# Kernel tuning notes

Hardware: AMD Instinct MI355X
Metric: run time of the kernel (lower is better)

Reference implementation:

```python
import jax, jax.numpy as jnp
import numpy as np

N = 50000   # nodes
E = 600000  # edges (avg degree 12)
F = 16      # raw node features
P = 32      # n_channels_preproc
C = 128     # n_channels
L = 6       # n_gnn_layers
LBL = 2     # n_labels


def _dense_init(k, fan_in, shape):
    return (jax.random.normal(k, shape, jnp.float32) / np.float32(np.sqrt(fan_in)))


def setup_inputs() -> dict:
    key = jax.random.key(0)
    ks = jax.random.split(key, 12)
    return {
        "x": jax.random.normal(ks[0], (N, F), jnp.float32),
        "edge_src": jax.random.randint(ks[1], (E,), 0, N, dtype=jnp.int32),
        "edge_dst": jax.random.randint(ks[2], (E,), 0, N, dtype=jnp.int32),
        "edge_weight": jax.random.uniform(ks[3], (E,), jnp.float32),  # normalized-adjacency values
        "preproc_W": _dense_init(ks[4], F, (F, P)), "preproc_b": jnp.zeros((P,), jnp.float32),
        "fc_in1_W": _dense_init(ks[5], P, (P, C)), "fc_in1_b": jnp.zeros((C,), jnp.float32),
        "fc_in2_W": _dense_init(ks[6], P, (P, C)), "fc_in2_b": jnp.zeros((C,), jnp.float32),
        "gcn_W": _dense_init(ks[7], C, (L, C, C)), "gcn_b": jnp.zeros((L, C), jnp.float32),
        "fcg_W": _dense_init(ks[8], 2 * C, (L, 2 * C, C)), "fcg_b": jnp.zeros((L, C), jnp.float32),
        "last1_W": _dense_init(ks[9], 2 * C, (2 * C, C)), "last1_b": jnp.zeros((C,), jnp.float32),
        "last2_W": _dense_init(ks[10], C, (C, LBL)), "last2_b": jnp.zeros((LBL,), jnp.float32),
    }


def reference(x, edge_src, edge_dst, edge_weight,
              preproc_W, preproc_b, fc_in1_W, fc_in1_b, fc_in2_W, fc_in2_b,
              gcn_W, gcn_b, fcg_W, fcg_b, last1_W, last1_b, last2_W, last2_b):
    relu = jax.nn.relu
    h = relu(x @ preproc_W + preproc_b)                      # preproc Dense
    node_id = relu(h @ fc_in1_W + fc_in1_b)                  # node identity branch
    h = relu(h @ fc_in2_W + fc_in2_b)

    def layer(h, params):
        W, b, Wf, bf = params
        # GCNConv: act(A_hat @ (h @ W) + b), A_hat as COO edge list
        hw = h @ W                                           # [N, C]
        msg = hw[edge_src] * edge_weight[:, None]            # [E, C]
        agg = jax.ops.segment_sum(msg, edge_dst, num_segments=N)
        g = relu(agg + b)
        merged = jnp.concatenate([node_id, g], axis=-1)      # [N, 2C]
        return relu(merged @ Wf + bf), None                  # dropout = identity (eval)

    h, _ = jax.lax.scan(layer, h, (gcn_W, gcn_b, fcg_W, fcg_b))

    merged = jnp.concatenate([node_id, h], axis=-1)
    h = relu(merged @ last1_W + last1_b)
    return jax.nn.sigmoid(h @ last2_W + last2_b)             # [N, n_labels]
```

## Files before the change

kernel.cpp:

```cpp
#include <hip/hip_runtime.h>
#include <cstddef>
#include <cstdint>

#define NN 50000
#define NE 600000
#define NB 391

typedef __attribute__((ext_vector_type(8))) short bf16x8;
typedef __attribute__((ext_vector_type(4))) float f32x4;

#define SWZ(x) (((x) ^ ((x) >> 2)) & 3)

__device__ __forceinline__ float bf2f(ushort u) {
    return __uint_as_float(((uint32_t)u) << 16);
}
__device__ __forceinline__ ushort f2bf(float f) {
    uint32_t b = __float_as_uint(f);
    return (ushort)((b + 0x7FFF + ((b >> 16) & 1)) >> 16);
}

__global__ __launch_bounds__(256)
void convert_weights(const float* __restrict__ f1W, const float* __restrict__ f2W,
                     const float* __restrict__ gW, const float* __restrict__ fgW,
                     const float* __restrict__ l1W, ushort* __restrict__ wt)
{
    int i = blockIdx.x * 256 + threadIdx.x;
    if (i >= 335872) return;
    float v;
    if (i < 4096) {
        int c = i >> 5, k = i & 31;
        v = f1W[k * 128 + c];
    } else if (i < 8192) {
        int j = i - 4096; int c = j >> 5, k = j & 31;
        v = f2W[k * 128 + c];
    } else if (i < 8192 + 98304) {
        int j = i - 8192; int l = j >> 14, r = j & 16383;
        int c = r >> 7, k = r & 127;
        v = gW[l * 16384 + k * 128 + c];
    } else if (i < 8192 + 98304 + 196608) {
        int j = i - (8192 + 98304); int l = j >> 15, r = j & 32767;
        int c = r >> 8, k = r & 255;
        v = fgW[l * 32768 + k * 128 + c];
    } else {
        int j = i - (8192 + 98304 + 196608);
        int c = j >> 8, k = j & 255;
        v = l1W[k * 128 + c];
    }
    wt[i] = f2bf(v);
}

__global__ __launch_bounds__(256)
void preproc_kernel(const float* __restrict__ x, const float* __restrict__ W,
                    const float* __restrict__ b, ushort* __restrict__ out)
{
    __shared__ float Wl[512];
    __shared__ float bl[32];
    int tx = threadIdx.x;
    Wl[tx]       = W[tx];
    Wl[tx + 256] = W[tx + 256];
    if (tx < 32) bl[tx] = b[tx];
    __syncthreads();
    int n = blockIdx.x * 256 + tx;
    if (n >= NN) return;
    float xr[16];
    const float4* xp = (const float4*)(x + (size_t)n * 16);
#pragma unroll
    for (int q = 0; q < 4; ++q) {
        float4 v = xp[q];
        xr[q*4+0]=v.x; xr[q*4+1]=v.y; xr[q*4+2]=v.z; xr[q*4+3]=v.w;
    }
    float acc[32];
#pragma unroll
    for (int c = 0; c < 32; ++c) acc[c] = bl[c];
#pragma unroll
    for (int k = 0; k < 16; ++k)
#pragma unroll
        for (int c = 0; c < 32; ++c)
            acc[c] = fmaf(xr[k], Wl[k*32+c], acc[c]);
    ushort4* op = (ushort4*)(out + (size_t)n * 32);
#pragma unroll
    for (int q = 0; q < 8; ++q) {
        ushort4 v;
        v.x = f2bf(fmaxf(acc[q*4+0], 0.f));
        v.y = f2bf(fmaxf(acc[q*4+1], 0.f));
        v.z = f2bf(fmaxf(acc[q*4+2], 0.f));
        v.w = f2bf(fmaxf(acc[q*4+3], 0.f));
        op[q] = v;
    }
}

__global__ __launch_bounds__(128)
void gemm_mfma(const ushort* __restrict__ A1, int K1,
               const ushort* __restrict__ Wt, const float* __restrict__ bias,
               ushort* __restrict__ out, int nrows)
{
    __shared__ ushort Atile[64 * 32];
    __shared__ ushort Btile[128 * 32];
    const int tx   = threadIdx.x;
    const int wave = tx >> 6;
    const int lane = tx & 63;
    const int bm   = blockIdx.x * 64;
    const int Ktot = K1;

    const int rs  = lane >> 2;
    const int chn = (lane & 3) ^ SWZ(rs);
    const int m    = lane & 15;
    const int quad = lane >> 4;
    const int slot = quad ^ SWZ(m);

    f32x4 acc0[8], acc1[8];
#pragma unroll
    for (int t = 0; t < 8; ++t) {
        acc0[t] = (f32x4){0.f, 0.f, 0.f, 0.f};
        acc1[t] = (f32x4){0.f, 0.f, 0.f, 0.f};
    }

    for (int kk = 0; kk < Ktot; kk += 32) {
#pragma unroll
        for (int i = 0; i < 2; ++i) {
            int seg = wave + 2 * i;
            int row = seg * 16 + rs;
            int ar  = bm + row; if (ar >= nrows) ar = nrows - 1;
            __builtin_amdgcn_global_load_lds(
                (const __attribute__((address_space(1))) void*)
                    (A1 + (size_t)ar * K1 + kk + chn * 8),
                (__attribute__((address_space(3))) void*)(Atile + seg * 512),
                16, 0, 0);
        }
#pragma unroll
        for (int i = 0; i < 4; ++i) {
            int seg = wave + 2 * i;
            int col = seg * 16 + rs;
            __builtin_amdgcn_global_load_lds(
                (const __attribute__((address_space(1))) void*)
                    (Wt + (size_t)col * Ktot + kk + chn * 8),
                (__attribute__((address_space(3))) void*)(Btile + seg * 512),
                16, 0, 0);
        }
        __syncthreads();
        bf16x8 af0 = *(const bf16x8*)(Atile + (wave * 32 + m) * 32 + slot * 8);
        bf16x8 af1 = *(const bf16x8*)(Atile + (wave * 32 + 16 + m) * 32 + slot * 8);
#pragma unroll
        for (int t = 0; t < 8; ++t) {
            bf16x8 bfr = *(const bf16x8*)(Btile + (t * 16 + m) * 32 + slot * 8);
            acc0[t] = __builtin_amdgcn_mfma_f32_16x16x32_bf16(af0, bfr, acc0[t], 0, 0, 0);
            acc1[t] = __builtin_amdgcn_mfma_f32_16x16x32_bf16(af1, bfr, acc1[t], 0, 0, 0);
        }
        __syncthreads();
    }

#pragma unroll
    for (int half = 0; half < 2; ++half) {
        const int orow0 = bm + wave * 32 + half * 16 + quad * 4;
#pragma unroll
        for (int t = 0; t < 8; ++t) {
            int col = t * 16 + m;
            float bb = bias[col];
            f32x4 a = half ? acc1[t] : acc0[t];
#pragma unroll
            for (int r = 0; r < 4; ++r) {
                int row = orow0 + r;
                if (row < nrows)
                    out[(size_t)row * 128 + col] = f2bf(fmaxf(a[r] + bb, 0.f));
            }
        }
    }
}

__global__ __launch_bounds__(128)
void gemm_fused(const ushort* __restrict__ A1, int K1,
                const ushort* __restrict__ A2, int K2,
                const ushort* __restrict__ Wt, const float* __restrict__ bias,
                const ushort* __restrict__ Wg,
                ushort* __restrict__ out_hw, int nrows)
{
    __shared__ ushort Atile[64 * 32];
    __shared__ ushort Btile[128 * 32];
    __shared__ ushort Xt[64 * 128];
    const int tx   = threadIdx.x;
    const int wave = tx >> 6;
    const int lane = tx & 63;
    const int bm   = blockIdx.x * 64;
    const int Ktot = K1 + K2;

    const int rs  = lane >> 2;
    const int chn = (lane & 3) ^ SWZ(rs);
    const int m    = lane & 15;
    const int quad = lane >> 4;
    const int slot = quad ^ SWZ(m);

    f32x4 acc0[8], acc1[8];
#pragma unroll
    for (int t = 0; t < 8; ++t) {
        acc0[t] = (f32x4){0.f, 0.f, 0.f, 0.f};
        acc1[t] = (f32x4){0.f, 0.f, 0.f, 0.f};
    }

    for (int kk = 0; kk < Ktot; kk += 32) {
        const ushort* asrc; int astr, kl;
        if (kk < K1) { asrc = A1; astr = K1; kl = kk; }
        else         { asrc = A2; astr = K2; kl = kk - K1; }
#pragma unroll
        for (int i = 0; i < 2; ++i) {
            int seg = wave + 2 * i;
            int row = seg * 16 + rs;
            int ar  = bm + row; if (ar >= nrows) ar = nrows - 1;
            __builtin_amdgcn_global_load_lds(
                (const __attribute__((address_space(1))) void*)
                    (asrc + (size_t)ar * astr + kl + chn * 8),
                (__attribute__((address_space(3))) void*)(Atile + seg * 512),
                16, 0, 0);
        }
#pragma unroll
        for (int i = 0; i < 4; ++i) {
            int seg = wave + 2 * i;
            int col = seg * 16 + rs;
            __builtin_amdgcn_global_load_lds(
                (const __attribute__((address_space(1))) void*)
                    (Wt + (size_t)col * Ktot + kk + chn * 8),
                (__attribute__((address_space(3))) void*)(Btile + seg * 512),
                16, 0, 0);
        }
        __syncthreads();
        bf16x8 af0 = *(const bf16x8*)(Atile + (wave * 32 + m) * 32 + slot * 8);
        bf16x8 af1 = *(const bf16x8*)(Atile + (wave * 32 + 16 + m) * 32 + slot * 8);
#pragma unroll
        for (int t = 0; t < 8; ++t) {
            bf16x8 bfr = *(const bf16x8*)(Btile + (t * 16 + m) * 32 + slot * 8);
            acc0[t] = __builtin_amdgcn_mfma_f32_16x16x32_bf16(af0, bfr, acc0[t], 0, 0, 0);
            acc1[t] = __builtin_amdgcn_mfma_f32_16x16x32_bf16(af1, bfr, acc1[t], 0, 0, 0);
        }
        __syncthreads();
    }

#pragma unroll
    for (int half = 0; half < 2; ++half) {
        int rbase = wave * 32 + half * 16 + quad * 4;
#pragma unroll
        for (int t = 0; t < 8; ++t) {
            int col = t * 16 + m;
            float bb = bias[col];
            int c32 = col >> 5, within = col & 7, ks = (col >> 3) & 3;
            f32x4 a = half ? acc1[t] : acc0[t];
#pragma unroll
            for (int r = 0; r < 4; ++r) {
                int row = rbase + r;
                int pos = ks ^ SWZ(row & 15);
                Xt[row * 128 + c32 * 32 + pos * 8 + within] =
                    f2bf(fmaxf(a[r] + bb, 0.f));
            }
        }
    }
#pragma unroll
    for (int t = 0; t < 8; ++t) {
        acc0[t] = (f32x4){0.f, 0.f, 0.f, 0.f};
        acc1[t] = (f32x4){0.f, 0.f, 0.f, 0.f};
    }
    __syncthreads();

    for (int c32 = 0; c32 < 4; ++c32) {
        int kk = c32 * 32;
#pragma unroll
        for (int i = 0; i < 4; ++i) {
            int seg = wave + 2 * i;
            int col = seg * 16 + rs;
            __builtin_amdgcn_global_load_lds(
                (const __attribute__((address_space(1))) void*)
                    (Wg + (size_t)col * 128 + kk + chn * 8),
                (__attribute__((address_space(3))) void*)(Btile + seg * 512),
                16, 0, 0);
        }
        __syncthreads();
        bf16x8 af0 = *(const bf16x8*)(Xt + (wave * 32 + m) * 128 + kk + slot * 8);
        bf16x8 af1 = *(const bf16x8*)(Xt + (wave * 32 + 16 + m) * 128 + kk + slot * 8);
#pragma unroll
        for (int t = 0; t < 8; ++t) {
            bf16x8 bfr = *(const bf16x8*)(Btile + (t * 16 + m) * 32 + slot * 8);
            acc0[t] = __builtin_amdgcn_mfma_f32_16x16x32_bf16(af0, bfr, acc0[t], 0, 0, 0);
            acc1[t] = __builtin_amdgcn_mfma_f32_16x16x32_bf16(af1, bfr, acc1[t], 0, 0, 0);
        }
        __syncthreads();
    }

#pragma unroll
    for (int half = 0; half < 2; ++half) {
        const int orow0 = bm + wave * 32 + half * 16 + quad * 4;
#pragma unroll
        for (int t = 0; t < 8; ++t) {
            int col = t * 16 + m;
            f32x4 a = half ? acc1[t] : acc0[t];
#pragma unroll
            for (int r = 0; r < 4; ++r) {
                int row = orow0 + r;
                if (row < nrows)
                    out_hw[(size_t)row * 128 + col] = f2bf(a[r]);
            }
        }
    }
}

__global__ __launch_bounds__(128)
void gemm_last(const ushort* __restrict__ nid, const ushort* __restrict__ agg,
               const ushort* __restrict__ Wt, const float* __restrict__ bias5,
               const ushort* __restrict__ Wl1, const float* __restrict__ l1b,
               const float* __restrict__ l2W, const float* __restrict__ l2b,
               float* __restrict__ out, int nrows)
{
    __shared__ ushort Atile[64 * 32];
    __shared__ ushort Btile[128 * 32];
    __shared__ ushort Xt[64 * 128];
    __shared__ float  w2s[256];
    const int tx   = threadIdx.x;
    const int wave = tx >> 6;
    const int lane = tx & 63;
    const int bm   = blockIdx.x * 64;

    w2s[tx]       = l2W[tx];
    w2s[tx + 128] = l2W[tx + 128];

    const int rs  = lane >> 2;
    const int chn = (lane & 3) ^ SWZ(rs);
    const int m    = lane & 15;
    const int quad = lane >> 4;
    const int slot = quad ^ SWZ(m);

    f32x4 acc0[8], acc1[8];
#pragma unroll
    for (int t = 0; t < 8; ++t) {
        acc0[t] = (f32x4){0.f, 0.f, 0.f, 0.f};
        acc1[t] = (f32x4){0.f, 0.f, 0.f, 0.f};
    }

    for (int kk = 0; kk < 256; kk += 32) {
        const ushort* asrc; int kl;
        if (kk < 128) { asrc = nid; kl = kk; }
        else          { asrc = agg; kl = kk - 128; }
#pragma unroll
        for (int i = 0; i < 2; ++i) {
            int seg = wave + 2 * i;
            int row = seg * 16 + rs;
            int ar  = bm + row; if (ar >= nrows) ar = nrows - 1;
            __builtin_amdgcn_global_load_lds(
                (const __attribute__((address_space(1))) void*)
                    (asrc + (size_t)ar * 128 + kl + chn * 8),
                (__attribute__((address_space(3))) void*)(Atile + seg * 512),
                16, 0, 0);
        }
#pragma unroll
        for (int i = 0; i < 4; ++i) {
            int seg = wave + 2 * i;
            int col = seg * 16 + rs;
            __builtin_amdgcn_global_load_lds(
                (const __attribute__((address_space(1))) void*)
                    (Wt + (size_t)col * 256 + kk + chn * 8),
                (__attribute__((address_space(3))) void*)(Btile + seg * 512),
                16, 0, 0);
        }
        __syncthreads();
        bf16x8 af0 = *(const bf16x8*)(Atile + (wave * 32 + m) * 32 + slot * 8);
        bf16x8 af1 = *(const bf16x8*)(Atile + (wave * 32 + 16 + m) * 32 + slot * 8);
#pragma unroll
        for (int t = 0; t < 8; ++t) {
            bf16x8 bfr = *(const bf16x8*)(Btile + (t * 16 + m) * 32 + slot * 8);
            acc0[t] = __builtin_amdgcn_mfma_f32_16x16x32_bf16(af0, bfr, acc0[t], 0, 0, 0);
            acc1[t] = __builtin_amdgcn_mfma_f32_16x16x32_bf16(af1, bfr, acc1[t], 0, 0, 0);
        }
        __syncthreads();
    }

#pragma unroll
    for (int half = 0; half < 2; ++half) {
        int rbase = wave * 32 + half * 16 + quad * 4;
#pragma unroll
        for (int t = 0; t < 8; ++t) {
            int col = t * 16 + m;
            float bb = bias5[col];
            int c32 = col >> 5, within = col & 7, ks = (col >> 3) & 3;
            f32x4 a = half ? acc1[t] : acc0[t];
#pragma unroll
            for (int r = 0; r < 4; ++r) {
                int row = rbase + r;
                int pos = ks ^ SWZ(row & 15);
                Xt[row * 128 + c32 * 32 + pos * 8 + within] =
                    f2bf(fmaxf(a[r] + bb, 0.f));
            }
        }
    }
#pragma unroll
    for (int t = 0; t < 8; ++t) {
        acc0[t] = (f32x4){0.f, 0.f, 0.f, 0.f};
        acc1[t] = (f32x4){0.f, 0.f, 0.f, 0.f};
    }
    __syncthreads();

    for (int c8 = 0; c8 < 8; ++c8) {
        int kk = c8 * 32;
        if (c8 < 4) {
#pragma unroll
            for (int i = 0; i < 2; ++i) {
                int seg = wave + 2 * i;
                int row = seg * 16 + rs;
                int ar  = bm + row; if (ar >= nrows) ar = nrows - 1;
                __builtin_amdgcn_global_load_lds(
                    (const __attribute__((address_space(1))) void*)
                        (nid + (size_t)ar * 128 + kk + chn * 8),
                    (__attribute__((address_space(3))) void*)(Atile + seg * 512),
                    16, 0, 0);
            }
        }
#pragma unroll
        for (int i = 0; i < 4; ++i) {
            int seg = wave + 2 * i;
            int col = seg * 16 + rs;
            __builtin_amdgcn_global_load_lds(
                (const __attribute__((address_space(1))) void*)
                    (Wl1 + (size_t)col * 256 + kk + chn * 8),
                (__attribute__((address_space(3))) void*)(Btile + seg * 512),
                16, 0, 0);
        }
        __syncthreads();
        bf16x8 af0, af1;
        if (c8 < 4) {
            af0 = *(const bf16x8*)(Atile + (wave * 32 + m) * 32 + slot * 8);
            af1 = *(const bf16x8*)(Atile + (wave * 32 + 16 + m) * 32 + slot * 8);
        } else {
            int ko = (c8 - 4) * 32;
            af0 = *(const bf16x8*)(Xt + (wave * 32 + m) * 128 + ko + slot * 8);
            af1 = *(const bf16x8*)(Xt + (wave * 32 + 16 + m) * 128 + ko + slot * 8);
        }
#pragma unroll
        for (int t = 0; t < 8; ++t) {
            bf16x8 bfr = *(const bf16x8*)(Btile + (t * 16 + m) * 32 + slot * 8);
            acc0[t] = __builtin_amdgcn_mfma_f32_16x16x32_bf16(af0, bfr, acc0[t], 0, 0, 0);
            acc1[t] = __builtin_amdgcn_mfma_f32_16x16x32_bf16(af1, bfr, acc1[t], 0, 0, 0);
        }
        __syncthreads();
    }

    float bb[8];
#pragma unroll
    for (int t = 0; t < 8; ++t) bb[t] = l1b[t * 16 + m];
    float b20 = l2b[0], b21 = l2b[1];
#pragma unroll
    for (int half = 0; half < 2; ++half) {
#pragma unroll
        for (int r = 0; r < 4; ++r) {
            float p0 = 0.f, p1 = 0.f;
#pragma unroll
            for (int t = 0; t < 8; ++t) {
                int col = t * 16 + m;
                f32x4 a = half ? acc1[t] : acc0[t];
                float v = fmaxf(a[r] + bb[t], 0.f);
                p0 = fmaf(v, w2s[col * 2 + 0], p0);
                p1 = fmaf(v, w2s[col * 2 + 1], p1);
            }
#pragma unroll
            for (int mask = 1; mask < 16; mask <<= 1) {
                p0 += __shfl_xor(p0, mask);
                p1 += __shfl_xor(p1, mask);
            }
            if (m == 0) {
                int row = bm + wave * 32 + half * 16 + quad * 4 + r;
                if (row < nrows) {
                    out[(size_t)row * 2 + 0] = 1.f / (1.f + __expf(-(p0 + b20)));
                    out[(size_t)row * 2 + 1] = 1.f / (1.f + __expf(-(p1 + b21)));
                }
            }
        }
    }
}


__global__ __launch_bounds__(256)
void bhist_kernel(const int* __restrict__ dst, int* __restrict__ bcnt)
{
    __shared__ int h[NB];
    int tx = threadIdx.x;
    for (int i = tx; i < NB; i += 256) h[i] = 0;
    __syncthreads();
    int e0 = blockIdx.x * 1024;
#pragma unroll
    for (int k = 0; k < 4; ++k) {
        int e = e0 + k * 256 + tx;
        if (e < NE) atomicAdd(&h[dst[e] >> 7], 1);
    }
    __syncthreads();
    for (int i = tx; i < NB; i += 256)
        if (h[i]) atomicAdd(&bcnt[i], h[i]);
}

__global__ __launch_bounds__(512)
void bscan_kernel(const int* __restrict__ bcnt, int* __restrict__ bbase,
                  int* __restrict__ bcur)
{
    __shared__ int buf[512];
    int t = threadIdx.x;
    int v = (t < NB) ? bcnt[t] : 0;
    buf[t] = v;
    __syncthreads();
    for (int s = 1; s < 512; s <<= 1) {
        int u = (t >= s) ? buf[t - s] : 0;
        __syncthreads();
        buf[t] += u;
        __syncthreads();
    }
    if (t < NB) {
        int ex = buf[t] - v;
        bbase[t] = ex;
        bcur[t]  = ex;
    }
    if (t == 0) bbase[NB] = NE;
}

__global__ __launch_bounds__(256)
void pass1_kernel(const int* __restrict__ src, const int* __restrict__ dst,
                  const float* __restrict__ w, int* __restrict__ bcur,
                  unsigned int* __restrict__ stage_pk,
                  unsigned char* __restrict__ stage_dl)
{
    __shared__ int cnt[NB];
    __shared__ int gbase[NB];
    int tx = threadIdx.x;
    for (int i = tx; i < NB; i += 256) cnt[i] = 0;
    __syncthreads();
    int e0 = blockIdx.x * 1024;
    int myd[4], myrank[4];
    unsigned int mypk[4];
#pragma unroll
    for (int k = 0; k < 4; ++k) {
        int e = e0 + k * 256 + tx;
        if (e < NE) {
            int d = dst[e];
            myd[k]    = d;
            mypk[k]   = (unsigned int)src[e] | ((unsigned int)f2bf(w[e]) << 17);
            myrank[k] = atomicAdd(&cnt[d >> 7], 1);
        } else {
            myd[k] = -1;
        }
    }
    __syncthreads();
    for (int i = tx; i < NB; i += 256)
        gbase[i] = cnt[i] ? atomicAdd(&bcur[i], cnt[i]) : 0;
    __syncthreads();
#pragma unroll
    for (int k = 0; k < 4; ++k) {
        if (myd[k] >= 0) {
            int p = gbase[myd[k] >> 7] + myrank[k];
            stage_pk[p] = mypk[k];
            stage_dl[p] = (unsigned char)(myd[k] & 127);
        }
    }
}

__global__ __launch_bounds__(256)
void pass2_kernel(const unsigned int* __restrict__ stage_pk,
                  const unsigned char* __restrict__ stage_dl,
                  const int* __restrict__ bbase,
                  unsigned int* __restrict__ esw, int* __restrict__ off)
{
    __shared__ int h[128];
    __shared__ int lofs[128];
    int b    = blockIdx.x;
    int tx   = threadIdx.x;
    int base = bbase[b];
    int cnt  = bbase[b + 1] - base;
    if (tx < 128) h[tx] = 0;
    __syncthreads();
    for (int i = tx; i < cnt; i += 256)
        atomicAdd(&h[stage_dl[base + i]], 1);
    __syncthreads();
    if (tx == 0) {
        int run = 0;
        for (int i = 0; i < 128; ++i) { lofs[i] = run; run += h[i]; }
    }
    __syncthreads();
    int node0 = b * 128;
    if (tx < 128) {
        int n = node0 + tx;
        if (n < NN) off[n] = base + lofs[tx];
        h[tx] = 0;
    }
    if (b == NB - 1 && tx == 0) off[NN] = NE;
    __syncthreads();
    for (int i = tx; i < cnt; i += 256) {
        int d = stage_dl[base + i];
        int r = atomicAdd(&h[d], 1);
        esw[base + lofs[d] + r] = stage_pk[base + i];
    }
}

__global__ __launch_bounds__(256)
void gather_agg(const ushort* __restrict__ hw,
                const unsigned int* __restrict__ esw,
                const int* __restrict__ off, const float* __restrict__ gbias,
                ushort* __restrict__ agg)
{
    const int g    = blockIdx.x * 4 + (threadIdx.x >> 6);
    const int lane = threadIdx.x & 63;
    int n = g * 8;
    if (n >= NN) return;
    int n_end = n + 8; if (n_end > NN) n_end = NN;
    const int base = off[n];
    const int end  = off[n_end];
    int nb = off[n + 1];
    const ushort* hp = hw + lane * 2;
    const float g0 = gbias[lane * 2], g1 = gbias[lane * 2 + 1];
    float a0 = 0.f, a1 = 0.f;

    for (int chunk = base; chunk < end; chunk += 64) {
        int idx = chunk + lane;
        int pk = (idx < end) ? (int)esw[idx] : 0;
        int cnt = end - chunk; if (cnt > 64) cnt = 64;
        int cnt8 = (cnt + 7) & ~7;
        for (int j = 0; j < cnt8; j += 8) {
            int pp[8];
            unsigned int rv[8];
#pragma unroll
            for (int k = 0; k < 8; ++k)
                pp[k] = __builtin_amdgcn_readlane(pk, j + k);
#pragma unroll
            for (int k = 0; k < 8; ++k)
                rv[k] = *(const unsigned int*)(hp + (size_t)(pp[k] & 0x1FFFF) * 128);
#pragma unroll
            for (int k = 0; k < 8; ++k) {
                int e = chunk + j + k;
                while (e == nb) {
                    unsigned int o = (unsigned int)f2bf(fmaxf(a0 + g0, 0.f)) |
                                     ((unsigned int)f2bf(fmaxf(a1 + g1, 0.f)) << 16);
                    *(unsigned int*)(agg + (size_t)n * 128 + lane * 2) = o;
                    a0 = 0.f; a1 = 0.f;
                    ++n;
                    nb = (n < n_end) ? off[n + 1] : 0x7fffffff;
                }
                float w = bf2f((ushort)((unsigned int)pp[k] >> 17));
                a0 = fmaf(bf2f((ushort)(rv[k] & 0xffff)), w, a0);
                a1 = fmaf(bf2f((ushort)(rv[k] >> 16)),    w, a1);
            }
        }
    }
    while (n < n_end) {
        unsigned int o = (unsigned int)f2bf(fmaxf(a0 + g0, 0.f)) |
                         ((unsigned int)f2bf(fmaxf(a1 + g1, 0.f)) << 16);
        *(unsigned int*)(agg + (size_t)n * 128 + lane * 2) = o;
        a0 = 0.f; a1 = 0.f;
        ++n;
    }
}

extern "C" void kernel_launch(void* const* d_in, const int* in_sizes, int n_in,
                              void* d_out, int out_size, void* d_ws, size_t ws_size,
                              hipStream_t stream)
{
    const float* x    = (const float*)d_in[0];
    const int*   esrc = (const int*)  d_in[1];
    const int*   edst = (const int*)  d_in[2];
    const float* ew   = (const float*)d_in[3];
    const float* preW = (const float*)d_in[4];
    const float* preb = (const float*)d_in[5];
    const float* f1W  = (const float*)d_in[6];
    const float* f1b  = (const float*)d_in[7];
    const float* f2W  = (const float*)d_in[8];
    const float* f2b  = (const float*)d_in[9];
    const float* gW   = (const float*)d_in[10];
    const float* gb   = (const float*)d_in[11];
    const float* fgW  = (const float*)d_in[12];
    const float* fgb  = (const float*)d_in[13];
    const float* l1W  = (const float*)d_in[14];
    const float* l1b  = (const float*)d_in[15];
    const float* l2W  = (const float*)d_in[16];
    const float* l2b  = (const float*)d_in[17];
    float* out = (float*)d_out;

    ushort* wt   = (ushort*)d_ws;
    ushort* wf1  = wt;
    ushort* wf2  = wf1 + 4096;
    ushort* wg   = wf2 + 4096;
    ushort* wfg  = wg  + 98304;
    ushort* wl1  = wfg + 196608;
    ushort* h0b  = wl1 + 32768;
    ushort* nidb = h0b  + (size_t)NN * 32;
    ushort* hwb  = nidb + (size_t)NN * 128;
    ushort* aggb = hwb  + (size_t)NN * 128;
    ushort* endu = aggb + (size_t)NN * 128;
    unsigned int* esw      = (unsigned int*)(((uintptr_t)endu + 15) & ~(uintptr_t)15);
    unsigned int* stage_pk = esw + NE;
    int*          bcnt     = (int*)(stage_pk + NE);
    int*          bbase    = bcnt + NB + 1;
    int*          bcur     = bbase + NB + 1;
    int*          off      = bcur + NB + 1;
    unsigned char* stage_dl = (unsigned char*)(off + NN + 2);

    const int gblocks = (NN + 63) / 64;
    const int eblocks = (NE + 1023) / 1024;
    const int ngroups = (NN + 7) / 8;
    const int wblocks = (ngroups + 3) / 4;

    convert_weights<<<(335872 + 255) / 256, 256, 0, stream>>>(f1W, f2W, gW, fgW, l1W, wt);

    hipMemsetAsync(bcnt, 0, (size_t)NB * sizeof(int), stream);
    bhist_kernel<<<eblocks, 256, 0, stream>>>(edst, bcnt);
    bscan_kernel<<<1, 512, 0, stream>>>(bcnt, bbase, bcur);
    pass1_kernel<<<eblocks, 256, 0, stream>>>(esrc, edst, ew, bcur, stage_pk, stage_dl);
    pass2_kernel<<<NB, 256, 0, stream>>>(stage_pk, stage_dl, bbase, esw, off);

    preproc_kernel<<<(NN + 255) / 256, 256, 0, stream>>>(x, preW, preb, h0b);
    gemm_mfma<<<gblocks, 128, 0, stream>>>(h0b, 32, wf1, f1b, nidb, NN);
    gemm_fused<<<gblocks, 128, 0, stream>>>(h0b, 32, nullptr, 0, wf2, f2b,
                                            wg, hwb, NN);
    for (int l = 0; l < 6; ++l) {
        gather_agg<<<wblocks, 256, 0, stream>>>(hwb, esw, off,
                                                gb + (size_t)l * 128, aggb);
        if (l < 5) {
            gemm_fused<<<gblocks, 128, 0, stream>>>(nidb, 128, aggb, 128,
                                                    wfg + (size_t)l * 32768,
                                                    fgb + (size_t)l * 128,
                                                    wg + (size_t)(l + 1) * 16384,
                                                    hwb, NN);
        }
    }
    gemm_last<<<gblocks, 128, 0, stream>>>(nidb, aggb,
                                           wfg + (size_t)5 * 32768,
                                           fgb + (size_t)5 * 128,
                                           wl1, l1b, l2W, l2b, out, NN);
}
```

Baseline: 428.1 us.

## Fuse edge gather-aggregation into the per-layer GEMM via LDS staging

The separate gather_agg kernel is removed. Each GEMM block now aggregates neighbour messages for its own 64 rows straight into a swizzled LDS tile, which then serves as the second half of the K dimension. hw buffers are ping-ponged because the gather reads the previous layer's hw while the new hw is written. This removes a launch per layer and the global write and read of the agg tensor, at the cost of 16KB more LDS per block (lower occupancy) and gather work spread over only 128-thread blocks, with two waves each handling 32 nodes serially.

```diff
diff --git a/kernel.cpp b/kernel.cpp
--- a/kernel.cpp
+++ b/kernel.cpp
@@ -169,7 +169,6 @@
 
 __global__ __launch_bounds__(128)
 void gemm_fused(const ushort* __restrict__ A1, int K1,
-                const ushort* __restrict__ A2, int K2,
                 const ushort* __restrict__ Wt, const float* __restrict__ bias,
                 const ushort* __restrict__ Wg,
                 ushort* __restrict__ out_hw, int nrows)
@@ -181,7 +180,7 @@
     const int wave = tx >> 6;
     const int lane = tx & 63;
     const int bm   = blockIdx.x * 64;
-    const int Ktot = K1 + K2;
+    const int Ktot = K1;
 
     const int rs  = lane >> 2;
     const int chn = (lane & 3) ^ SWZ(rs);
@@ -197,9 +196,6 @@
     }
 
     for (int kk = 0; kk < Ktot; kk += 32) {
-        const ushort* asrc; int astr, kl;
-        if (kk < K1) { asrc = A1; astr = K1; kl = kk; }
-        else         { asrc = A2; astr = K2; kl = kk - K1; }
 #pragma unroll
         for (int i = 0; i < 2; ++i) {
             int seg = wave + 2 * i;
@@ -207,7 +203,7 @@
             int ar  = bm + row; if (ar >= nrows) ar = nrows - 1;
             __builtin_amdgcn_global_load_lds(
                 (const __attribute__((address_space(1))) void*)
-                    (asrc + (size_t)ar * astr + kl + chn * 8),
+                    (A1 + (size_t)ar * K1 + kk + chn * 8),
                 (__attribute__((address_space(3))) void*)(Atile + seg * 512),
                 16, 0, 0);
         }
@@ -299,24 +295,78 @@
     }
 }
 
+#define GATHER_TO_LDS(AggL)                                                     \
+    {                                                                           \
+        int n0 = bm + wave * 32;                                                \
+        if (n0 < nrows) {                                                       \
+            int n_end = n0 + 32; if (n_end > nrows) n_end = nrows;              \
+            const int base = off[n0];                                           \
+            const int end  = off[n_end];                                        \
+            int nb = off[n0 + 1];                                               \
+            int n  = n0;                                                        \
+            const ushort* hp = hw + lane * 2;                                   \
+            const float g0 = gbias[lane * 2], g1 = gbias[lane * 2 + 1];         \
+            const int c32w = lane >> 4, ksw = (lane >> 2) & 3, wi2 = lane & 3;  \
+            float a0 = 0.f, a1 = 0.f;                                           \
+            for (int chunk = base; chunk < end; chunk += 64) {                  \
+                int idx = chunk + lane;                                         \
+                int pk = (idx < end) ? (int)esw[idx] : 0;                       \
+                int cnt = end - chunk; if (cnt > 64) cnt = 64;                  \
+                int cnt8 = (cnt + 7) & ~7;                                      \
+                for (int j = 0; j < cnt8; j += 8) {                             \
+                    int pp[8]; unsigned int rv[8];                              \
+                    _Pragma("unroll")                                           \
+                    for (int k = 0; k < 8; ++k)                                 \
+                        pp[k] = __builtin_amdgcn_readlane(pk, j + k);           \
+                    _Pragma("unroll")                                           \
+                    for (int k = 0; k < 8; ++k)                                 \
+                        rv[k] = *(const unsigned int*)(hp + (size_t)(pp[k] & 0x1FFFF) * 128); \
+                    _Pragma("unroll")                                           \
+                    for (int k = 0; k < 8; ++k) {                               \
+                        int e = chunk + j + k;                                  \
+                        while (e == nb) {                                       \
+                            int row = n - bm;                                   \
+                            int pos = ksw ^ SWZ(row & 15);                      \
+                            unsigned int o = (unsigned int)f2bf(fmaxf(a0 + g0, 0.f)) | \
+                                ((unsigned int)f2bf(fmaxf(a1 + g1, 0.f)) << 16);\
+                            ((unsigned int*)(AggL))[row * 64 + c32w * 16 + pos * 4 + wi2] = o; \
+                            a0 = 0.f; a1 = 0.f; ++n;                            \
+                            nb = (n < n_end) ? off[n + 1] : 0x7fffffff;         \
+                        }                                                       \
+                        float w = bf2f((ushort)((unsigned int)pp[k] >> 17));    \
+                        a0 = fmaf(bf2f((ushort)(rv[k] & 0xffff)), w, a0);       \
+                        a1 = fmaf(bf2f((ushort)(rv[k] >> 16)),    w, a1);       \
+                    }                                                           \
+                }                                                               \
+            }                                                                   \
+            while (n < n_end) {                                                 \
+                int row = n - bm;                                               \
+                int pos = ksw ^ SWZ(row & 15);                                  \
+                unsigned int o = (unsigned int)f2bf(fmaxf(a0 + g0, 0.f)) |      \
+                    ((unsigned int)f2bf(fmaxf(a1 + g1, 0.f)) << 16);            \
+                ((unsigned int*)(AggL))[row * 64 + c32w * 16 + pos * 4 + wi2] = o; \
+                a0 = 0.f; a1 = 0.f; ++n;                                        \
+            }                                                                   \
+        }                                                                       \
+    }
+
 __global__ __launch_bounds__(128)
-void gemm_last(const ushort* __restrict__ nid, const ushort* __restrict__ agg,
-               const ushort* __restrict__ Wt, const float* __restrict__ bias5,
-               const ushort* __restrict__ Wl1, const float* __restrict__ l1b,
-               const float* __restrict__ l2W, const float* __restrict__ l2b,
-               float* __restrict__ out, int nrows)
+void gemm_fused_g(const ushort* __restrict__ hw,
+                  const unsigned int* __restrict__ esw,
+                  const int* __restrict__ off, const float* __restrict__ gbias,
+                  const ushort* __restrict__ nid,
+                  const ushort* __restrict__ Wt, const float* __restrict__ bias,
+                  const ushort* __restrict__ Wg,
+                  ushort* __restrict__ out_hw, int nrows)
 {
     __shared__ ushort Atile[64 * 32];
     __shared__ ushort Btile[128 * 32];
     __shared__ ushort Xt[64 * 128];
-    __shared__ float  w2s[256];
+    __shared__ ushort AggL[64 * 128];
     const int tx   = threadIdx.x;
     const int wave = tx >> 6;
     const int lane = tx & 63;
     const int bm   = blockIdx.x * 64;
-
-    w2s[tx]       = l2W[tx];
-    w2s[tx + 128] = l2W[tx + 128];
 
     const int rs  = lane >> 2;
     const int chn = (lane & 3) ^ SWZ(rs);
@@ -324,6 +374,9 @@
     const int quad = lane >> 4;
     const int slot = quad ^ SWZ(m);
 
+    GATHER_TO_LDS(AggL)
+    __syncthreads();
+
     f32x4 acc0[8], acc1[8];
 #pragma unroll
     for (int t = 0; t < 8; ++t) {
@@ -332,70 +385,7 @@
     }
 
     for (int kk = 0; kk < 256; kk += 32) {
-        const ushort* asrc; int kl;
-        if (kk < 128) { asrc = nid; kl = kk; }
-        else          { asrc = agg; kl = kk - 128; }
-#pragma unroll
-        for (int i = 0; i < 2; ++i) {
-            int seg = wave + 2 * i;
-            int row = seg * 16 + rs;
-            int ar  = bm + row; if (ar >= nrows) ar = nrows - 1;
-            __builtin_amdgcn_global_load_lds(
-                (const __attribute__((address_space(1))) void*)
-                    (asrc + (size_t)ar * 128 + kl + chn * 8),
-                (__attribute__((address_space(3))) void*)(Atile + seg * 512),
-                16, 0, 0);
-        }
-#pragma unroll
-        for (int i = 0; i < 4; ++i) {
-            int seg = wave + 2 * i;
-            int col = seg * 16 + rs;
-            __builtin_amdgcn_global_load_lds(
-                (const __attribute__((address_space(1))) void*)
-                    (Wt + (size_t)col * 256 + kk + chn * 8),
-                (__attribute__((address_space(3))) void*)(Btile + seg * 512),
-                16, 0, 0);
-        }
-        __syncthreads();
-        bf16x8 af0 = *(const bf16x8*)(Atile + (wave * 32 + m) * 32 + slot * 8);
-        bf16x8 af1 = *(const bf16x8*)(Atile + (wave * 32 + 16 + m) * 32 + slot * 8);
-#pragma unroll
-        for (int t = 0; t < 8; ++t) {
-            bf16x8 bfr = *(const bf16x8*)(Btile + (t * 16 + m) * 32 + slot * 8);
-            acc0[t] = __builtin_amdgcn_mfma_f32_16x16x32_bf16(af0, bfr, acc0[t], 0, 0, 0);
-            acc1[t] = __builtin_amdgcn_mfma_f32_16x16x32_bf16(af1, bfr, acc1[t], 0, 0, 0);
-        }
-        __syncthreads();
-    }
-
-#pragma unroll
-    for (int half = 0; half < 2; ++half) {
-        int rbase = wave * 32 + half * 16 + quad * 4;
-#pragma unroll
-        for (int t = 0; t < 8; ++t) {
-            int col = t * 16 + m;
-            float bb = bias5[col];
-            int c32 = col >> 5, within = col & 7, ks = (col >> 3) & 3;
-            f32x4 a = half ? acc1[t] : acc0[t];
-#pragma unroll
-            for (int r = 0; r < 4; ++r) {
-                int row = rbase + r;
-                int pos = ks ^ SWZ(row & 15);
-                Xt[row * 128 + c32 * 32 + pos * 8 + within] =
-                    f2bf(fmaxf(a[r] + bb, 0.f));
-            }
-        }
-    }
-#pragma unroll
-    for (int t = 0; t < 8; ++t) {
-        acc0[t] = (f32x4){0.f, 0.f, 0.f, 0.f};
-        acc1[t] = (f32x4){0.f, 0.f, 0.f, 0.f};
-    }
-    __syncthreads();
-
-    for (int c8 = 0; c8 < 8; ++c8) {
-        int kk = c8 * 32;
-        if (c8 < 4) {
+        if (kk < 128) {
 #pragma unroll
             for (int i = 0; i < 2; ++i) {
                 int seg = wave + 2 * i;
@@ -414,6 +404,223 @@
             int col = seg * 16 + rs;
             __builtin_amdgcn_global_load_lds(
                 (const __attribute__((address_space(1))) void*)
+                    (Wt + (size_t)col * 256 + kk + chn * 8),
+                (__attribute__((address_space(3))) void*)(Btile + seg * 512),
+                16, 0, 0);
+        }
+        __syncthreads();
+        bf16x8 af0, af1;
+        if (kk < 128) {
+            af0 = *(const bf16x8*)(Atile + (wave * 32 + m) * 32 + slot * 8);
+            af1 = *(const bf16x8*)(Atile + (wave * 32 + 16 + m) * 32 + slot * 8);
+        } else {
+            int ko = kk - 128;
+            af0 = *(const bf16x8*)(AggL + (wave * 32 + m) * 128 + ko + slot * 8);
+            af1 = *(const bf16x8*)(AggL + (wave * 32 + 16 + m) * 128 + ko + slot * 8);
+        }
+#pragma unroll
+        for (int t = 0; t < 8; ++t) {
+            bf16x8 bfr = *(const bf16x8*)(Btile + (t * 16 + m) * 32 + slot * 8);
+            acc0[t] = __builtin_amdgcn_mfma_f32_16x16x32_bf16(af0, bfr, acc0[t], 0, 0, 0);
+            acc1[t] = __builtin_amdgcn_mfma_f32_16x16x32_bf16(af1, bfr, acc1[t], 0, 0, 0);
+        }
+        __syncthreads();
+    }
+
+#pragma unroll
+    for (int half = 0; half < 2; ++half) {
+        int rbase = wave * 32 + half * 16 + quad * 4;
+#pragma unroll
+        for (int t = 0; t < 8; ++t) {
+            int col = t * 16 + m;
+            float bb = bias[col];
+            int c32 = col >> 5, within = col & 7, ks = (col >> 3) & 3;
+            f32x4 a = half ? acc1[t] : acc0[t];
+#pragma unroll
+            for (int r = 0; r < 4; ++r) {
+                int row = rbase + r;
+                int pos = ks ^ SWZ(row & 15);
+                Xt[row * 128 + c32 * 32 + pos * 8 + within] =
+                    f2bf(fmaxf(a[r] + bb, 0.f));
+            }
+        }
+    }
+#pragma unroll
+    for (int t = 0; t < 8; ++t) {
+        acc0[t] = (f32x4){0.f, 0.f, 0.f, 0.f};
+        acc1[t] = (f32x4){0.f, 0.f, 0.f, 0.f};
+    }
+    __syncthreads();
+
+    for (int c32 = 0; c32 < 4; ++c32) {
+        int kk = c32 * 32;
+#pragma unroll
+        for (int i = 0; i < 4; ++i) {
+            int seg = wave + 2 * i;
+            int col = seg * 16 + rs;
+            __builtin_amdgcn_global_load_lds(
+                (const __attribute__((address_space(1))) void*)
+                    (Wg + (size_t)col * 128 + kk + chn * 8),
+                (__attribute__((address_space(3))) void*)(Btile + seg * 512),
+                16, 0, 0);
+        }
+        __syncthreads();
+        bf16x8 af0 = *(const bf16x8*)(Xt + (wave * 32 + m) * 128 + kk + slot * 8);
+        bf16x8 af1 = *(const bf16x8*)(Xt + (wave * 32 + 16 + m) * 128 + kk + slot * 8);
+#pragma unroll
+        for (int t = 0; t < 8; ++t) {
+            bf16x8 bfr = *(const bf16x8*)(Btile + (t * 16 + m) * 32 + slot * 8);
+            acc0[t] = __builtin_amdgcn_mfma_f32_16x16x32_bf16(af0, bfr, acc0[t], 0, 0, 0);
+            acc1[t] = __builtin_amdgcn_mfma_f32_16x16x32_bf16(af1, bfr, acc1[t], 0, 0, 0);
+        }
+        __syncthreads();
+    }
+
+#pragma unroll
+    for (int half = 0; half < 2; ++half) {
+        const int orow0 = bm + wave * 32 + half * 16 + quad * 4;
+#pragma unroll
+        for (int t = 0; t < 8; ++t) {
+            int col = t * 16 + m;
+            f32x4 a = half ? acc1[t] : acc0[t];
+#pragma unroll
+            for (int r = 0; r < 4; ++r) {
+                int row = orow0 + r;
+                if (row < nrows)
+                    out_hw[(size_t)row * 128 + col] = f2bf(a[r]);
+            }
+        }
+    }
+}
+
+__global__ __launch_bounds__(128)
+void gemm_last_g(const ushort* __restrict__ hw,
+                 const unsigned int* __restrict__ esw,
+                 const int* __restrict__ off, const float* __restrict__ gbias,
+                 const ushort* __restrict__ nid,
+                 const ushort* __restrict__ Wt, const float* __restrict__ bias5,
+                 const ushort* __restrict__ Wl1, const float* __restrict__ l1b,
+                 const float* __restrict__ l2W, const float* __restrict__ l2b,
+                 float* __restrict__ out, int nrows)
+{
+    __shared__ ushort Atile[64 * 32];
+    __shared__ ushort Btile[128 * 32];
+    __shared__ ushort Xt[64 * 128];
+    __shared__ ushort AggL[64 * 128];
+    __shared__ float  w2s[256];
+    const int tx   = threadIdx.x;
+    const int wave = tx >> 6;
+    const int lane = tx & 63;
+    const int bm   = blockIdx.x * 64;
+
+    w2s[tx]       = l2W[tx];
+    w2s[tx + 128] = l2W[tx + 128];
+
+    const int rs  = lane >> 2;
+    const int chn = (lane & 3) ^ SWZ(rs);
+    const int m    = lane & 15;
+    const int quad = lane >> 4;
+    const int slot = quad ^ SWZ(m);
+
+    GATHER_TO_LDS(AggL)
+    __syncthreads();
+
+    f32x4 acc0[8], acc1[8];
+#pragma unroll
+    for (int t = 0; t < 8; ++t) {
+        acc0[t] = (f32x4){0.f, 0.f, 0.f, 0.f};
+        acc1[t] = (f32x4){0.f, 0.f, 0.f, 0.f};
+    }
+
+    for (int kk = 0; kk < 256; kk += 32) {
+        if (kk < 128) {
+#pragma unroll
+            for (int i = 0; i < 2; ++i) {
+                int seg = wave + 2 * i;
+                int row = seg * 16 + rs;
+                int ar  = bm + row; if (ar >= nrows) ar = nrows - 1;
+                __builtin_amdgcn_global_load_lds(
+                    (const __attribute__((address_space(1))) void*)
+                        (nid + (size_t)ar * 128 + kk + chn * 8),
+                    (__attribute__((address_space(3))) void*)(Atile + seg * 512),
+                    16, 0, 0);
+            }
+        }
+#pragma unroll
+        for (int i = 0; i < 4; ++i) {
+            int seg = wave + 2 * i;
+            int col = seg * 16 + rs;
+            __builtin_amdgcn_global_load_lds(
+                (const __attribute__((address_space(1))) void*)
+                    (Wt + (size_t)col * 256 + kk + chn * 8),
+                (__attribute__((address_space(3))) void*)(Btile + seg * 512),
+                16, 0, 0);
+        }
+        __syncthreads();
+        bf16x8 af0, af1;
+        if (kk < 128) {
+            af0 = *(const bf16x8*)(Atile + (wave * 32 + m) * 32 + slot * 8);
+            af1 = *(const bf16x8*)(Atile + (wave * 32 + 16 + m) * 32 + slot * 8);
+        } else {
+            int ko = kk - 128;
+            af0 = *(const bf16x8*)(AggL + (wave * 32 + m) * 128 + ko + slot * 8);
+            af1 = *(const bf16x8*)(AggL + (wave * 32 + 16 + m) * 128 + ko + slot * 8);
+        }
+#pragma unroll
+        for (int t = 0; t < 8; ++t) {
+            bf16x8 bfr = *(const bf16x8*)(Btile + (t * 16 + m) * 32 + slot * 8);
+            acc0[t] = __builtin_amdgcn_mfma_f32_16x16x32_bf16(af0, bfr, acc0[t], 0, 0, 0);
+            acc1[t] = __builtin_amdgcn_mfma_f32_16x16x32_bf16(af1, bfr, acc1[t], 0, 0, 0);
+        }
+        __syncthreads();
+    }
+
+#pragma unroll
+    for (int half = 0; half < 2; ++half) {
+        int rbase = wave * 32 + half * 16 + quad * 4;
+#pragma unroll
+        for (int t = 0; t < 8; ++t) {
+            int col = t * 16 + m;
+            float bb = bias5[col];
+            int c32 = col >> 5, within = col & 7, ks = (col >> 3) & 3;
+            f32x4 a = half ? acc1[t] : acc0[t];
+#pragma unroll
+            for (int r = 0; r < 4; ++r) {
+                int row = rbase + r;
+                int pos = ks ^ SWZ(row & 15);
+                Xt[row * 128 + c32 * 32 + pos * 8 + within] =
+                    f2bf(fmaxf(a[r] + bb, 0.f));
+            }
+        }
+    }
+#pragma unroll
+    for (int t = 0; t < 8; ++t) {
+        acc0[t] = (f32x4){0.f, 0.f, 0.f, 0.f};
+        acc1[t] = (f32x4){0.f, 0.f, 0.f, 0.f};
+    }
+    __syncthreads();
+
+    for (int c8 = 0; c8 < 8; ++c8) {
+        int kk = c8 * 32;
+        if (c8 < 4) {
+#pragma unroll
+            for (int i = 0; i < 2; ++i) {
+                int seg = wave + 2 * i;
+                int row = seg * 16 + rs;
+                int ar  = bm + row; if (ar >= nrows) ar = nrows - 1;
+                __builtin_amdgcn_global_load_lds(
+                    (const __attribute__((address_space(1))) void*)
+                        (nid + (size_t)ar * 128 + kk + chn * 8),
+                    (__attribute__((address_space(3))) void*)(Atile + seg * 512),
+                    16, 0, 0);
+            }
+        }
+#pragma unroll
+        for (int i = 0; i < 4; ++i) {
+            int seg = wave + 2 * i;
+            int col = seg * 16 + rs;
+            __builtin_amdgcn_global_load_lds(
+                (const __attribute__((address_space(1))) void*)
                     (Wl1 + (size_t)col * 256 + kk + chn * 8),
                 (__attribute__((address_space(3))) void*)(Btile + seg * 512),
                 16, 0, 0);
@@ -469,7 +676,6 @@
         }
     }
 }
-
 
 __global__ __launch_bounds__(256)
 void bhist_kernel(const int* __restrict__ dst, int* __restrict__ bcnt)
@@ -586,64 +792,6 @@
         int d = stage_dl[base + i];
         int r = atomicAdd(&h[d], 1);
         esw[base + lofs[d] + r] = stage_pk[base + i];
-    }
-}
-
-__global__ __launch_bounds__(256)
-void gather_agg(const ushort* __restrict__ hw,
-                const unsigned int* __restrict__ esw,
-                const int* __restrict__ off, const float* __restrict__ gbias,
-                ushort* __restrict__ agg)
-{
-    const int g    = blockIdx.x * 4 + (threadIdx.x >> 6);
-    const int lane = threadIdx.x & 63;
-    int n = g * 8;
-    if (n >= NN) return;
-    int n_end = n + 8; if (n_end > NN) n_end = NN;
-    const int base = off[n];
-    const int end  = off[n_end];
-    int nb = off[n + 1];
-    const ushort* hp = hw + lane * 2;
-    const float g0 = gbias[lane * 2], g1 = gbias[lane * 2 + 1];
-    float a0 = 0.f, a1 = 0.f;
-
-    for (int chunk = base; chunk < end; chunk += 64) {
-        int idx = chunk + lane;
-        int pk = (idx < end) ? (int)esw[idx] : 0;
-        int cnt = end - chunk; if (cnt > 64) cnt = 64;
-        int cnt8 = (cnt + 7) & ~7;
-        for (int j = 0; j < cnt8; j += 8) {
-            int pp[8];
-            unsigned int rv[8];
-#pragma unroll
-            for (int k = 0; k < 8; ++k)
-                pp[k] = __builtin_amdgcn_readlane(pk, j + k);
-#pragma unroll
-            for (int k = 0; k < 8; ++k)
-                rv[k] = *(const unsigned int*)(hp + (size_t)(pp[k] & 0x1FFFF) * 128);
-#pragma unroll
-            for (int k = 0; k < 8; ++k) {
-                int e = chunk + j + k;
-                while (e == nb) {
-                    unsigned int o = (unsigned int)f2bf(fmaxf(a0 + g0, 0.f)) |
-                                     ((unsigned int)f2bf(fmaxf(a1 + g1, 0.f)) << 16);
-                    *(unsigned int*)(agg + (size_t)n * 128 + lane * 2) = o;
-                    a0 = 0.f; a1 = 0.f;
-                    ++n;
-                    nb = (n < n_end) ? off[n + 1] : 0x7fffffff;
-                }
-                float w = bf2f((ushort)((unsigned int)pp[k] >> 17));
-                a0 = fmaf(bf2f((ushort)(rv[k] & 0xffff)), w, a0);
-                a1 = fmaf(bf2f((ushort)(rv[k] >> 16)),    w, a1);
-            }
-        }
-    }
-    while (n < n_end) {
-        unsigned int o = (unsigned int)f2bf(fmaxf(a0 + g0, 0.f)) |
-                         ((unsigned int)f2bf(fmaxf(a1 + g1, 0.f)) << 16);
-        *(unsigned int*)(agg + (size_t)n * 128 + lane * 2) = o;
-        a0 = 0.f; a1 = 0.f;
-        ++n;
     }
 }
 
@@ -679,9 +827,9 @@
     ushort* wl1  = wfg + 196608;
     ushort* h0b  = wl1 + 32768;
     ushort* nidb = h0b  + (size_t)NN * 32;
-    ushort* hwb  = nidb + (size_t)NN * 128;
-    ushort* aggb = hwb  + (size_t)NN * 128;
-    ushort* endu = aggb + (size_t)NN * 128;
+    ushort* hwA  = nidb + (size_t)NN * 128;
+    ushort* hwB  = hwA  + (size_t)NN * 128;
+    ushort* endu = hwB  + (size_t)NN * 128;
     unsigned int* esw      = (unsigned int*)(((uintptr_t)endu + 15) & ~(uintptr_t)15);
     unsigned int* stage_pk = esw + NE;
     int*          bcnt     = (int*)(stage_pk + NE);
@@ -692,8 +840,6 @@
 
     const int gblocks = (NN + 63) / 64;
     const int eblocks = (NE + 1023) / 1024;
-    const int ngroups = (NN + 7) / 8;
-    const int wblocks = (ngroups + 3) / 4;
 
     convert_weights<<<(335872 + 255) / 256, 256, 0, stream>>>(f1W, f2W, gW, fgW, l1W, wt);
 
@@ -705,21 +851,21 @@
 
     preproc_kernel<<<(NN + 255) / 256, 256, 0, stream>>>(x, preW, preb, h0b);
     gemm_mfma<<<gblocks, 128, 0, stream>>>(h0b, 32, wf1, f1b, nidb, NN);
-    gemm_fused<<<gblocks, 128, 0, stream>>>(h0b, 32, nullptr, 0, wf2, f2b,
-                                            wg, hwb, NN);
-    for (int l = 0; l < 6; ++l) {
-        gather_agg<<<wblocks, 256, 0, stream>>>(hwb, esw, off,
-                                                gb + (size_t)l * 128, aggb);
-        if (l < 5) {
-            gemm_fused<<<gblocks, 128, 0, stream>>>(nidb, 128, aggb, 128,
-                                                    wfg + (size_t)l * 32768,
-                                                    fgb + (size_t)l * 128,
-                                                    wg + (size_t)(l + 1) * 16384,
-                                                    hwb, NN);
-        }
-    }
-    gemm_last<<<gblocks, 128, 0, stream>>>(nidb, aggb,
-                                           wfg + (size_t)5 * 32768,
-                                           fgb + (size_t)5 * 128,
-                                           wl1, l1b, l2W, l2b, out, NN);
-}
+    gemm_fused<<<gblocks, 128, 0, stream>>>(h0b, 32, wf2, f2b, wg, hwA, NN);
+    ushort* hin = hwA;
+    ushort* hout = hwB;
+    for (int l = 0; l < 5; ++l) {
+        gemm_fused_g<<<gblocks, 128, 0, stream>>>(hin, esw, off,
+                                                  gb + (size_t)l * 128, nidb,
+                                                  wfg + (size_t)l * 32768,
+                                                  fgb + (size_t)l * 128,
+                                                  wg + (size_t)(l + 1) * 16384,
+                                                  hout, NN);
+        ushort* tmp = hin; hin = hout; hout = tmp;
+    }
+    gemm_last_g<<<gblocks, 128, 0, stream>>>(hin, esw, off,
+                                             gb + (size_t)5 * 128, nidb,
+                                             wfg + (size_t)5 * 32768,
+                                             fgb + (size_t)5 * 128,
+                                             wl1, l1b, l2W, l2b, out, NN);
+}
```

After: 787.9 us. 84.0% more time.
